# Kernel optimization log

Measured on AMD Instinct MI355X. Metric: run time of the kernel, lower is better.

The kernel has to match this reference:

```python
import jax, jax.numpy as jnp
import numpy as np

B, P1, P2 = 64, 15, 14            # batch, H/patch+1, W/patch
E0, E1, E2 = 8, 8, 8               # embed_dim per mode (512 total)
H1, H2, H3 = 2, 2, 2               # heads per mode (8 heads total)
X, Y, Z = E0 // H1, E1 // H2, E2 // H3  # per-head dims (4,4,4) -> head_dim 64
SCALE = (X * Y * Z) ** -0.5


def tle(x, W0, W1, W2, b):
    # mode-n products on last three modes (ignore_modes=(0,1,2)) + bias
    y = jnp.einsum('bpqxyz,ax->bpqayz', x, W0)
    y = jnp.einsum('bpqayz,cy->bpqacz', y, W1)
    y = jnp.einsum('bpqacz,dz->bpqacd', y, W2)
    return y + b


def split_heads(t):
    b, p, q = t.shape[:3]
    t = t.reshape(b, p, q, X, H1, Y, H2, Z, H3)
    return t.transpose(0, 1, 2, 4, 6, 8, 3, 5, 7)


def attention_core(x, Wq0, Wq1, Wq2, bq, Wk0, Wk1, Wk2, bk,
                   Wv0, Wv1, Wv2, bv, Wo0, Wo1, Wo2, bo):
    Q = split_heads(tle(x, Wq0, Wq1, Wq2, bq))
    K = split_heads(tle(x, Wk0, Wk1, Wk2, bk))
    V = split_heads(tle(x, Wv0, Wv1, Wv2, bv))
    # scores over spatial patch pairs per (h1,h2,h3) head triple
    attn = jnp.einsum('bpqdefxyz,bmndefxyz->bdefpqmn', Q, K) * SCALE
    b, d, e, f, p, q, m, n = attn.shape
    a = jax.nn.softmax(attn.reshape(b, d, e, f, p, q, m * n), axis=-1)
    a = a.reshape(b, d, e, f, p, q, m, n)
    o = jnp.einsum('bdefpqmn,bmndefxyz->bdefpqxyz', a, V)
    # b h1 h2 h3 p q x y z -> b p q (x h1)(y h2)(z h3)
    o = o.transpose(0, 4, 5, 6, 1, 7, 2, 8, 3).reshape(b, p, q, E0, E1, E2)
    return tle(o, Wo0, Wo1, Wo2, bo)


def setup_inputs() -> dict:
    key = jax.random.key(0)
    ks = jax.random.split(key, 17)
    inp = {'x': jax.random.normal(ks[0], (B, P1, P2, E0, E1, E2), jnp.float32)}
    i = 1
    for name in ('q', 'k', 'v', 'o'):
        for mode, dim in enumerate((E0, E1, E2)):
            inp[f'W{name}{mode}'] = jax.random.normal(ks[i], (dim, dim), jnp.float32) * 0.1
            i += 1
        inp[f'b{name}'] = jax.random.normal(ks[i], (E0, E1, E2), jnp.float32) * 0.02
        i += 1
    return inp


def reference(x, Wq0, Wq1, Wq2, bq, Wk0, Wk1, Wk2, bk,
              Wv0, Wv1, Wv2, bv, Wo0, Wo1, Wo2, bo):
    return attention_core(x, Wq0, Wq1, Wq2, bq, Wk0, Wk1, Wk2, bk,
                          Wv0, Wv1, Wv2, bv, Wo0, Wo1, Wo2, bo)
```

## Files before the change

### kernel.cpp

```cpp
#include <hip/hip_runtime.h>

typedef unsigned int   u32;
typedef unsigned short u16;
typedef float f32x16 __attribute__((ext_vector_type(16)));
typedef short s16x8  __attribute__((ext_vector_type(8)));
typedef u32   u32x4  __attribute__((ext_vector_type(4)));
typedef u32   u32x2  __attribute__((ext_vector_type(2)));

#define B_   64
#define P1_  15
#define P2_  14
#define S_   210
#define SP_  224
#define NT_  (B_*S_)
#define E_   512
#define NH_  8
#define HD_  64
#define KSC  0.18033688011112042f

__device__ __forceinline__ u16 f2bf(float f) {
    u32 u = __float_as_uint(f);
    u += 0x7fffu + ((u >> 16) & 1u);
    return (u16)(u >> 16);
}
__device__ __forceinline__ float bf2f(u16 h) {
    return __uint_as_float(((u32)h) << 16);
}
__device__ __forceinline__ u32 cvtpk(float lo, float hi) {
    u32 r;
    asm("v_cvt_pk_bf16_f32 %0, %1, %2" : "=v"(r) : "v"(lo), "v"(hi));
    return r;
}

__device__ __forceinline__ void wfence() {
    asm volatile("s_waitcnt lgkmcnt(0)" ::: "memory");
}

__device__ __forceinline__ void mode_proj(
        const float* xs, float* t1, float* t2,
        const float* __restrict__ W0, const float* __restrict__ W1,
        const float* __restrict__ W2, const float* __restrict__ bb,
        int t, float* y3)
{
    {
        float xv[8];
        #pragma unroll
        for (int i = 0; i < 8; ++i) xv[i] = xs[i*66 + t];
        #pragma unroll
        for (int a = 0; a < 8; ++a) {
            float acc = 0.f;
            #pragma unroll
            for (int i = 0; i < 8; ++i) acc = fmaf(W0[a*8+i], xv[i], acc);
            t1[a*68 + t] = acc;
        }
    }
    wfence();
    {
        const int a = t >> 3, z = t & 7;
        float yv[8];
        #pragma unroll
        for (int y = 0; y < 8; ++y) yv[y] = t1[a*68 + y*8 + z];
        #pragma unroll
        for (int c = 0; c < 8; ++c) {
            float acc = 0.f;
            #pragma unroll
            for (int y = 0; y < 8; ++y) acc = fmaf(W1[c*8+y], yv[y], acc);
            t2[(a*8 + c)*9 + z] = acc;
        }
    }
    wfence();
    {
        float zv[8];
        #pragma unroll
        for (int z = 0; z < 8; ++z) zv[z] = t2[t*9 + z];
        #pragma unroll
        for (int d = 0; d < 8; ++d) {
            float acc = bb[t*8 + d];
            #pragma unroll
            for (int z = 0; z < 8; ++z) acc = fmaf(W2[d*8+z], zv[z], acc);
            y3[d] = acc;
        }
    }
    wfence();
}

__global__ __launch_bounds__(512) void k_qkv(
    const float* __restrict__ x,
    const float* __restrict__ Wq0, const float* __restrict__ Wq1,
    const float* __restrict__ Wq2, const float* __restrict__ bq,
    const float* __restrict__ Wk0, const float* __restrict__ Wk1,
    const float* __restrict__ Wk2, const float* __restrict__ bk,
    const float* __restrict__ Wv0, const float* __restrict__ Wv1,
    const float* __restrict__ Wv2, const float* __restrict__ bv,
    u16* __restrict__ Qo, u16* __restrict__ Ko, u16* __restrict__ Vo)
{
    __shared__ float xs[8][528];
    __shared__ float t1[8][544];
    __shared__ float t2[8][576];
    const int w = threadIdx.x >> 6, t = threadIdx.x & 63;
    const int tok = blockIdx.x*8 + w;
    const int b   = tok / S_;
    const int s   = tok - b * S_;

    const float* xp = x + (size_t)tok * E_;
    #pragma unroll
    for (int k4 = 0; k4 < 2; ++k4) {
        const float4 vv = *reinterpret_cast<const float4*>(xp + k4*256 + t*4);
        const int m0 = k4*4 + (t >> 4);
        const int in = (t*4) & 63;
        xs[w][m0*66 + in + 0] = vv.x;
        xs[w][m0*66 + in + 1] = vv.y;
        xs[w][m0*66 + in + 2] = vv.z;
        xs[w][m0*66 + in + 3] = vv.w;
    }
    wfence();

    const int a  = t >> 3, c = t & 7;
    const int x_ = a >> 1, h1 = a & 1;
    const int y_ = c >> 1, h2 = c & 1;

    float y3[8];

    mode_proj(xs[w], t1[w], t2[w], Wq0, Wq1, Wq2, bq, t, y3);
    #pragma unroll
    for (int h3 = 0; h3 < 2; ++h3) {
        const int h = (((h1 << 1) | h2) << 1) | h3;
        u32x2 pk;
        pk[0] = cvtpk(y3[0 + h3], y3[2 + h3]);
        pk[1] = cvtpk(y3[4 + h3], y3[6 + h3]);
        *reinterpret_cast<u32x2*>(
            Qo + ((size_t)(b*NH_ + h)*SP_ + s)*HD_ + (x_*16 + y_*4)) = pk;
    }
    mode_proj(xs[w], t1[w], t2[w], Wk0, Wk1, Wk2, bk, t, y3);
    #pragma unroll
    for (int h3 = 0; h3 < 2; ++h3) {
        const int h = (((h1 << 1) | h2) << 1) | h3;
        u32x2 pk;
        pk[0] = cvtpk(y3[0 + h3], y3[2 + h3]);
        pk[1] = cvtpk(y3[4 + h3], y3[6 + h3]);
        *reinterpret_cast<u32x2*>(
            Ko + ((size_t)(b*NH_ + h)*SP_ + s)*HD_ + (x_*16 + y_*4)) = pk;
    }
    mode_proj(xs[w], t1[w], t2[w], Wv0, Wv1, Wv2, bv, t, y3);
    #pragma unroll
    for (int h3 = 0; h3 < 2; ++h3) {
        const int h = (((h1 << 1) | h2) << 1) | h3;
        u32x2 pk;
        pk[0] = cvtpk(y3[0 + h3], y3[2 + h3]);
        pk[1] = cvtpk(y3[4 + h3], y3[6 + h3]);
        *reinterpret_cast<u32x2*>(
            Vo + ((size_t)(b*NH_ + h)*SP_ + s)*HD_ + (x_*16 + y_*4)) = pk;
    }
}

__global__ __launch_bounds__(512, 2) void k_attn(
    const u16* __restrict__ Q, const u16* __restrict__ K,
    const u16* __restrict__ V, u16* __restrict__ O)
{
    __shared__ u16   Kl[SP_*64];
    __shared__ u16   Vt[64*232];
    __shared__ float invl[8*32];

    const int bh  = blockIdx.x;
    const int tid = threadIdx.x;
    const u16* Qg = Q + (size_t)bh*SP_*HD_;
    const u16* Kg = K + (size_t)bh*SP_*HD_;
    const u16* Vg = V + (size_t)bh*SP_*HD_;

    const int w    = tid >> 6;
    const int lane = tid & 63;
    const int l31  = lane & 31;
    const int hi   = lane >> 5;
    const int strip = (w < 7) ? w : 6;

    const u16* qb = Qg + (size_t)(strip*32 + l31)*64 + hi*8;
    const s16x8 qf0 = *(const s16x8*)(qb +  0);
    const s16x8 qf1 = *(const s16x8*)(qb + 16);
    const s16x8 qf2 = *(const s16x8*)(qb + 32);
    const s16x8 qf3 = *(const s16x8*)(qb + 48);

    #pragma unroll
    for (int i = 0; i < 4; ++i) {
        int sIdx = i*512 + tid;
        if (sIdx < 1792) {
            int row = sIdx >> 3, cc = sIdx & 7;
            u32x4 d = *(const u32x4*)(Kg + sIdx*8);
            *(u32x4*)&Kl[row*64 + (cc ^ (row & 7))*8] = d;
        }
    }
    if (tid < 448) {
        int tokg = tid >> 3, dg = tid & 7;
        int t0 = tokg*4, d0 = dg*8;
        u32x4 r0 = *(const u32x4*)(Vg + (size_t)(t0+0)*64 + d0);
        u32x4 r1 = *(const u32x4*)(Vg + (size_t)(t0+1)*64 + d0);
        u32x4 r2 = *(const u32x4*)(Vg + (size_t)(t0+2)*64 + d0);
        u32x4 r3 = *(const u32x4*)(Vg + (size_t)(t0+3)*64 + d0);
        #pragma unroll
        for (int j = 0; j < 8; ++j) {
            u32 sel = (j & 1) ? 0x07060302u : 0x05040100u;
            u32 lo  = __builtin_amdgcn_perm(r1[j>>1], r0[j>>1], sel);
            u32 hi2 = __builtin_amdgcn_perm(r3[j>>1], r2[j>>1], sel);
            *(u32x2*)&Vt[(d0+j)*232 + t0] = (u32x2){lo, hi2};
        }
    }
    __syncthreads();

    if (w >= 7) return;

    f32x16 oacc0 = {}, oacc1 = {};
    float  psum  = 0.f;
    const int swz = l31 & 7;

    #pragma unroll
    for (int kt = 0; kt < 7; ++kt) {
        const u16* kbase = &Kl[(kt*32 + l31)*64];
        f32x16 sacc = {};
        s16x8 kf0 = *(const s16x8*)(kbase + ((0 + hi) ^ swz)*8);
        s16x8 kf1 = *(const s16x8*)(kbase + ((2 + hi) ^ swz)*8);
        s16x8 kf2 = *(const s16x8*)(kbase + ((4 + hi) ^ swz)*8);
        s16x8 kf3 = *(const s16x8*)(kbase + ((6 + hi) ^ swz)*8);
        __builtin_amdgcn_s_setprio(1);
        sacc = __builtin_amdgcn_mfma_f32_32x32x16_bf16(kf0, qf0, sacc, 0, 0, 0);
        sacc = __builtin_amdgcn_mfma_f32_32x32x16_bf16(kf1, qf1, sacc, 0, 0, 0);
        sacc = __builtin_amdgcn_mfma_f32_32x32x16_bf16(kf2, qf2, sacc, 0, 0, 0);
        sacc = __builtin_amdgcn_mfma_f32_32x32x16_bf16(kf3, qf3, sacc, 0, 0, 0);
        __builtin_amdgcn_s_setprio(0);

        float p[16];
        #pragma unroll
        for (int r = 0; r < 16; ++r) p[r] = exp2f(sacc[r] * KSC);
        if (kt == 6) {
            const float hm = hi ? 0.f : 1.f;
            p[8] *= hm; p[9] *= hm;
            p[10] = 0.f; p[11] = 0.f; p[12] = 0.f; p[13] = 0.f; p[14] = 0.f; p[15] = 0.f;
        }
        #pragma unroll
        for (int r = 0; r < 16; ++r) psum += p[r];

        u32 c0, c1, c2, c3, c4, c5, c6, c7;
        asm("v_cvt_pk_bf16_f32 %0, %1, %2" : "=v"(c0) : "v"(p[0]),  "v"(p[1]));
        asm("v_cvt_pk_bf16_f32 %0, %1, %2" : "=v"(c1) : "v"(p[2]),  "v"(p[3]));
        asm("v_cvt_pk_bf16_f32 %0, %1, %2" : "=v"(c2) : "v"(p[4]),  "v"(p[5]));
        asm("v_cvt_pk_bf16_f32 %0, %1, %2" : "=v"(c3) : "v"(p[6]),  "v"(p[7]));
        asm("v_cvt_pk_bf16_f32 %0, %1, %2" : "=v"(c4) : "v"(p[8]),  "v"(p[9]));
        asm("v_cvt_pk_bf16_f32 %0, %1, %2" : "=v"(c5) : "v"(p[10]), "v"(p[11]));
        asm("v_cvt_pk_bf16_f32 %0, %1, %2" : "=v"(c6) : "v"(p[12]), "v"(p[13]));
        asm("v_cvt_pk_bf16_f32 %0, %1, %2" : "=v"(c7) : "v"(p[14]), "v"(p[15]));
        asm("v_permlane32_swap_b32 %0, %1" : "+v"(c0), "+v"(c2));
        asm("v_permlane32_swap_b32 %0, %1" : "+v"(c1), "+v"(c3));
        asm("v_permlane32_swap_b32 %0, %1" : "+v"(c4), "+v"(c6));
        asm("v_permlane32_swap_b32 %0, %1" : "+v"(c5), "+v"(c7));
        const s16x8 pf0 = __builtin_bit_cast(s16x8, (u32x4){c0, c1, c2, c3});
        const s16x8 pf1 = __builtin_bit_cast(s16x8, (u32x4){c4, c5, c6, c7});

        const u16* vb = &Vt[kt*32 + hi*8];
        s16x8 vf0 = *(const s16x8*)(vb + (0*32 + l31)*232 +  0);
        s16x8 vf1 = *(const s16x8*)(vb + (0*32 + l31)*232 + 16);
        s16x8 vf2 = *(const s16x8*)(vb + (1*32 + l31)*232 +  0);
        s16x8 vf3 = *(const s16x8*)(vb + (1*32 + l31)*232 + 16);
        __builtin_amdgcn_s_setprio(1);
        oacc0 = __builtin_amdgcn_mfma_f32_32x32x16_bf16(pf0, vf0, oacc0, 0, 0, 0);
        oacc0 = __builtin_amdgcn_mfma_f32_32x32x16_bf16(pf1, vf1, oacc0, 0, 0, 0);
        oacc1 = __builtin_amdgcn_mfma_f32_32x32x16_bf16(pf0, vf2, oacc1, 0, 0, 0);
        oacc1 = __builtin_amdgcn_mfma_f32_32x32x16_bf16(pf1, vf3, oacc1, 0, 0, 0);
        __builtin_amdgcn_s_setprio(0);
    }

    float tot = psum + __shfl_xor(psum, 32, 64);
    invl[w*32 + l31] = 1.0f / tot;
    asm volatile("s_waitcnt lgkmcnt(0)" ::: "memory");

    u16* Ob = O + ((size_t)bh*S_ + strip*32)*HD_;
    #pragma unroll
    for (int r = 0; r < 16; ++r) {
        const int q = (r & 3) + 8*(r >> 2) + 4*hi;
        if (strip == 6 && q >= 18) continue;
        const float iv = invl[w*32 + q];
        Ob[(size_t)q*64 + l31]      = f2bf(oacc0[r] * iv);
        Ob[(size_t)q*64 + 32 + l31] = f2bf(oacc1[r] * iv);
    }
}

__global__ __launch_bounds__(512) void k_oproj(
    const u16* __restrict__ O,
    const float* __restrict__ Wo0, const float* __restrict__ Wo1,
    const float* __restrict__ Wo2, const float* __restrict__ bo,
    float* __restrict__ out)
{
    __shared__ float xs[8][528];
    __shared__ float t1[8][544];
    __shared__ float t2[8][576];
    const int w = threadIdx.x >> 6, t = threadIdx.x & 63;
    const int tok = blockIdx.x*8 + w;
    const int b   = tok / S_;
    const int s   = tok - b * S_;

    const int a  = t >> 3, c = t & 7;
    const int x_ = a >> 1, h1 = a & 1;
    const int y_ = c >> 1, h2 = c & 1;
    #pragma unroll
    for (int h3 = 0; h3 < 2; ++h3) {
        const int h = (((h1 << 1) | h2) << 1) | h3;
        const ushort4 v = *reinterpret_cast<const ushort4*>(
            O + ((size_t)(b*NH_ + h)*S_ + s)*HD_ + (x_*16 + y_*4));
        xs[w][a*66 + c*8 + 0 + h3] = bf2f(v.x);
        xs[w][a*66 + c*8 + 2 + h3] = bf2f(v.y);
        xs[w][a*66 + c*8 + 4 + h3] = bf2f(v.z);
        xs[w][a*66 + c*8 + 6 + h3] = bf2f(v.w);
    }
    wfence();

    float y3[8];
    mode_proj(xs[w], t1[w], t2[w], Wo0, Wo1, Wo2, bo, t, y3);

    float4* op = reinterpret_cast<float4*>(out + (size_t)tok * E_ + t * 8);
    float4 u0, u1;
    u0.x = y3[0]; u0.y = y3[1]; u0.z = y3[2]; u0.w = y3[3];
    u1.x = y3[4]; u1.y = y3[5]; u1.z = y3[6]; u1.w = y3[7];
    op[0] = u0;
    op[1] = u1;
}

extern "C" void kernel_launch(void* const* d_in, const int* in_sizes, int n_in,
                              void* d_out, int out_size, void* d_ws, size_t ws_size,
                              hipStream_t stream)
{
    const float* x   = (const float*)d_in[0];
    const float* Wq0 = (const float*)d_in[1];
    const float* Wq1 = (const float*)d_in[2];
    const float* Wq2 = (const float*)d_in[3];
    const float* bq  = (const float*)d_in[4];
    const float* Wk0 = (const float*)d_in[5];
    const float* Wk1 = (const float*)d_in[6];
    const float* Wk2 = (const float*)d_in[7];
    const float* bk  = (const float*)d_in[8];
    const float* Wv0 = (const float*)d_in[9];
    const float* Wv1 = (const float*)d_in[10];
    const float* Wv2 = (const float*)d_in[11];
    const float* bv  = (const float*)d_in[12];
    const float* Wo0 = (const float*)d_in[13];
    const float* Wo1 = (const float*)d_in[14];
    const float* Wo2 = (const float*)d_in[15];
    const float* bo  = (const float*)d_in[16];

    const size_t TP = (size_t)B_ * NH_ * SP_ * HD_;
    u16* Qs = (u16*)d_ws;
    u16* Ks = Qs + TP;
    u16* Vs = Ks + TP;
    u16* Os = Vs + TP;

    k_qkv<<<NT_/8, 512, 0, stream>>>(x, Wq0, Wq1, Wq2, bq,
                                     Wk0, Wk1, Wk2, bk,
                                     Wv0, Wv1, Wv2, bv, Qs, Ks, Vs);
    k_attn<<<B_*NH_, 512, 0, stream>>>(Qs, Ks, Vs, Os);
    k_oproj<<<NT_/8, 512, 0, stream>>>(Os, Wo0, Wo1, Wo2, bo, (float*)d_out);
}
```

Measured before the change: 152.9 us.

## Fuse QKV, attention and output projection into one cooperative persistent kernel

```diff
diff --git a/kernel.cpp b/kernel.cpp
--- a/kernel.cpp
+++ b/kernel.cpp
@@ -1,4 +1,7 @@
 #include <hip/hip_runtime.h>
+#include <hip/hip_cooperative_groups.h>
+
+namespace cg = cooperative_groups;
 
 typedef unsigned int   u32;
 typedef unsigned short u16;
@@ -18,6 +21,9 @@
 #define HD_  64
 #define KSC  0.18033688011112042f
 
+#define NBLK 256
+#define TPB  512
+
 __device__ __forceinline__ u16 f2bf(float f) {
     u32 u = __float_as_uint(f);
     u += 0x7fffu + ((u >> 16) & 1u);
@@ -84,274 +90,282 @@
     wfence();
 }
 
-__global__ __launch_bounds__(512) void k_qkv(
-    const float* __restrict__ x,
-    const float* __restrict__ Wq0, const float* __restrict__ Wq1,
-    const float* __restrict__ Wq2, const float* __restrict__ bq,
-    const float* __restrict__ Wk0, const float* __restrict__ Wk1,
-    const float* __restrict__ Wk2, const float* __restrict__ bk,
-    const float* __restrict__ Wv0, const float* __restrict__ Wv1,
-    const float* __restrict__ Wv2, const float* __restrict__ bv,
-    u16* __restrict__ Qo, u16* __restrict__ Ko, u16* __restrict__ Vo)
+struct KParams {
+    const float *x;
+    const float *Wq0, *Wq1, *Wq2, *bq;
+    const float *Wk0, *Wk1, *Wk2, *bk;
+    const float *Wv0, *Wv1, *Wv2, *bv;
+    const float *Wo0, *Wo1, *Wo2, *bo;
+    u16 *Qs, *Ks, *Vs, *Os;
+    float *out;
+};
+
+
+__global__ __launch_bounds__(TPB, 4) void k_fused(KParams p)
 {
-    __shared__ float xs[8][528];
-    __shared__ float t1[8][544];
-    __shared__ float t2[8][576];
-    const int w = threadIdx.x >> 6, t = threadIdx.x & 63;
-    const int tok = blockIdx.x*8 + w;
-    const int b   = tok / S_;
-    const int s   = tok - b * S_;
-
-    const float* xp = x + (size_t)tok * E_;
-    #pragma unroll
-    for (int k4 = 0; k4 < 2; ++k4) {
-        const float4 vv = *reinterpret_cast<const float4*>(xp + k4*256 + t*4);
-        const int m0 = k4*4 + (t >> 4);
-        const int in = (t*4) & 63;
-        xs[w][m0*66 + in + 0] = vv.x;
-        xs[w][m0*66 + in + 1] = vv.y;
-        xs[w][m0*66 + in + 2] = vv.z;
-        xs[w][m0*66 + in + 3] = vv.w;
-    }
-    wfence();
-
-    const int a  = t >> 3, c = t & 7;
-    const int x_ = a >> 1, h1 = a & 1;
-    const int y_ = c >> 1, h2 = c & 1;
-
-    float y3[8];
-
-    mode_proj(xs[w], t1[w], t2[w], Wq0, Wq1, Wq2, bq, t, y3);
-    #pragma unroll
-    for (int h3 = 0; h3 < 2; ++h3) {
-        const int h = (((h1 << 1) | h2) << 1) | h3;
-        u32x2 pk;
-        pk[0] = cvtpk(y3[0 + h3], y3[2 + h3]);
-        pk[1] = cvtpk(y3[4 + h3], y3[6 + h3]);
-        *reinterpret_cast<u32x2*>(
-            Qo + ((size_t)(b*NH_ + h)*SP_ + s)*HD_ + (x_*16 + y_*4)) = pk;
-    }
-    mode_proj(xs[w], t1[w], t2[w], Wk0, Wk1, Wk2, bk, t, y3);
-    #pragma unroll
-    for (int h3 = 0; h3 < 2; ++h3) {
-        const int h = (((h1 << 1) | h2) << 1) | h3;
-        u32x2 pk;
-        pk[0] = cvtpk(y3[0 + h3], y3[2 + h3]);
-        pk[1] = cvtpk(y3[4 + h3], y3[6 + h3]);
-        *reinterpret_cast<u32x2*>(
-            Ko + ((size_t)(b*NH_ + h)*SP_ + s)*HD_ + (x_*16 + y_*4)) = pk;
-    }
-    mode_proj(xs[w], t1[w], t2[w], Wv0, Wv1, Wv2, bv, t, y3);
-    #pragma unroll
-    for (int h3 = 0; h3 < 2; ++h3) {
-        const int h = (((h1 << 1) | h2) << 1) | h3;
-        u32x2 pk;
-        pk[0] = cvtpk(y3[0 + h3], y3[2 + h3]);
-        pk[1] = cvtpk(y3[4 + h3], y3[6 + h3]);
-        *reinterpret_cast<u32x2*>(
-            Vo + ((size_t)(b*NH_ + h)*SP_ + s)*HD_ + (x_*16 + y_*4)) = pk;
-    }
-}
-
-__global__ __launch_bounds__(512, 2) void k_attn(
-    const u16* __restrict__ Q, const u16* __restrict__ K,
-    const u16* __restrict__ V, u16* __restrict__ O)
-{
-    __shared__ u16   Kl[SP_*64];
-    __shared__ u16   Vt[64*232];
-    __shared__ float invl[8*32];
-
-    const int bh  = blockIdx.x;
-    const int tid = threadIdx.x;
-    const u16* Qg = Q + (size_t)bh*SP_*HD_;
-    const u16* Kg = K + (size_t)bh*SP_*HD_;
-    const u16* Vg = V + (size_t)bh*SP_*HD_;
-
+    __shared__ __align__(16) char smem[59392];
+    cg::grid_group grid = cg::this_grid();
+
+    const int bid  = blockIdx.x;
+    const int tid  = threadIdx.x;
     const int w    = tid >> 6;
-    const int lane = tid & 63;
-    const int l31  = lane & 31;
-    const int hi   = lane >> 5;
-    const int strip = (w < 7) ? w : 6;
-
-    const u16* qb = Qg + (size_t)(strip*32 + l31)*64 + hi*8;
-    const s16x8 qf0 = *(const s16x8*)(qb +  0);
-    const s16x8 qf1 = *(const s16x8*)(qb + 16);
-    const s16x8 qf2 = *(const s16x8*)(qb + 32);
-    const s16x8 qf3 = *(const s16x8*)(qb + 48);
-
-    #pragma unroll
-    for (int i = 0; i < 4; ++i) {
-        int sIdx = i*512 + tid;
-        if (sIdx < 1792) {
-            int row = sIdx >> 3, cc = sIdx & 7;
-            u32x4 d = *(const u32x4*)(Kg + sIdx*8);
-            *(u32x4*)&Kl[row*64 + (cc ^ (row & 7))*8] = d;
-        }
-    }
-    if (tid < 448) {
-        int tokg = tid >> 3, dg = tid & 7;
-        int t0 = tokg*4, d0 = dg*8;
-        u32x4 r0 = *(const u32x4*)(Vg + (size_t)(t0+0)*64 + d0);
-        u32x4 r1 = *(const u32x4*)(Vg + (size_t)(t0+1)*64 + d0);
-        u32x4 r2 = *(const u32x4*)(Vg + (size_t)(t0+2)*64 + d0);
-        u32x4 r3 = *(const u32x4*)(Vg + (size_t)(t0+3)*64 + d0);
-        #pragma unroll
-        for (int j = 0; j < 8; ++j) {
-            u32 sel = (j & 1) ? 0x07060302u : 0x05040100u;
-            u32 lo  = __builtin_amdgcn_perm(r1[j>>1], r0[j>>1], sel);
-            u32 hi2 = __builtin_amdgcn_perm(r3[j>>1], r2[j>>1], sel);
-            *(u32x2*)&Vt[(d0+j)*232 + t0] = (u32x2){lo, hi2};
-        }
-    }
-    __syncthreads();
-
-    if (w >= 7) return;
-
-    f32x16 oacc0 = {}, oacc1 = {};
-    float  psum  = 0.f;
-    const int swz = l31 & 7;
-
-    #pragma unroll
-    for (int kt = 0; kt < 7; ++kt) {
-        const u16* kbase = &Kl[(kt*32 + l31)*64];
-        f32x16 sacc = {};
-        s16x8 kf0 = *(const s16x8*)(kbase + ((0 + hi) ^ swz)*8);
-        s16x8 kf1 = *(const s16x8*)(kbase + ((2 + hi) ^ swz)*8);
-        s16x8 kf2 = *(const s16x8*)(kbase + ((4 + hi) ^ swz)*8);
-        s16x8 kf3 = *(const s16x8*)(kbase + ((6 + hi) ^ swz)*8);
-        __builtin_amdgcn_s_setprio(1);
-        sacc = __builtin_amdgcn_mfma_f32_32x32x16_bf16(kf0, qf0, sacc, 0, 0, 0);
-        sacc = __builtin_amdgcn_mfma_f32_32x32x16_bf16(kf1, qf1, sacc, 0, 0, 0);
-        sacc = __builtin_amdgcn_mfma_f32_32x32x16_bf16(kf2, qf2, sacc, 0, 0, 0);
-        sacc = __builtin_amdgcn_mfma_f32_32x32x16_bf16(kf3, qf3, sacc, 0, 0, 0);
-        __builtin_amdgcn_s_setprio(0);
-
-        float p[16];
-        #pragma unroll
-        for (int r = 0; r < 16; ++r) p[r] = exp2f(sacc[r] * KSC);
-        if (kt == 6) {
-            const float hm = hi ? 0.f : 1.f;
-            p[8] *= hm; p[9] *= hm;
-            p[10] = 0.f; p[11] = 0.f; p[12] = 0.f; p[13] = 0.f; p[14] = 0.f; p[15] = 0.f;
-        }
-        #pragma unroll
-        for (int r = 0; r < 16; ++r) psum += p[r];
-
-        u32 c0, c1, c2, c3, c4, c5, c6, c7;
-        asm("v_cvt_pk_bf16_f32 %0, %1, %2" : "=v"(c0) : "v"(p[0]),  "v"(p[1]));
-        asm("v_cvt_pk_bf16_f32 %0, %1, %2" : "=v"(c1) : "v"(p[2]),  "v"(p[3]));
-        asm("v_cvt_pk_bf16_f32 %0, %1, %2" : "=v"(c2) : "v"(p[4]),  "v"(p[5]));
-        asm("v_cvt_pk_bf16_f32 %0, %1, %2" : "=v"(c3) : "v"(p[6]),  "v"(p[7]));
-        asm("v_cvt_pk_bf16_f32 %0, %1, %2" : "=v"(c4) : "v"(p[8]),  "v"(p[9]));
-        asm("v_cvt_pk_bf16_f32 %0, %1, %2" : "=v"(c5) : "v"(p[10]), "v"(p[11]));
-        asm("v_cvt_pk_bf16_f32 %0, %1, %2" : "=v"(c6) : "v"(p[12]), "v"(p[13]));
-        asm("v_cvt_pk_bf16_f32 %0, %1, %2" : "=v"(c7) : "v"(p[14]), "v"(p[15]));
-        asm("v_permlane32_swap_b32 %0, %1" : "+v"(c0), "+v"(c2));
-        asm("v_permlane32_swap_b32 %0, %1" : "+v"(c1), "+v"(c3));
-        asm("v_permlane32_swap_b32 %0, %1" : "+v"(c4), "+v"(c6));
-        asm("v_permlane32_swap_b32 %0, %1" : "+v"(c5), "+v"(c7));
-        const s16x8 pf0 = __builtin_bit_cast(s16x8, (u32x4){c0, c1, c2, c3});
-        const s16x8 pf1 = __builtin_bit_cast(s16x8, (u32x4){c4, c5, c6, c7});
-
-        const u16* vb = &Vt[kt*32 + hi*8];
-        s16x8 vf0 = *(const s16x8*)(vb + (0*32 + l31)*232 +  0);
-        s16x8 vf1 = *(const s16x8*)(vb + (0*32 + l31)*232 + 16);
-        s16x8 vf2 = *(const s16x8*)(vb + (1*32 + l31)*232 +  0);
-        s16x8 vf3 = *(const s16x8*)(vb + (1*32 + l31)*232 + 16);
-        __builtin_amdgcn_s_setprio(1);
-        oacc0 = __builtin_amdgcn_mfma_f32_32x32x16_bf16(pf0, vf0, oacc0, 0, 0, 0);
-        oacc0 = __builtin_amdgcn_mfma_f32_32x32x16_bf16(pf1, vf1, oacc0, 0, 0, 0);
-        oacc1 = __builtin_amdgcn_mfma_f32_32x32x16_bf16(pf0, vf2, oacc1, 0, 0, 0);
-        oacc1 = __builtin_amdgcn_mfma_f32_32x32x16_bf16(pf1, vf3, oacc1, 0, 0, 0);
-        __builtin_amdgcn_s_setprio(0);
-    }
-
-    float tot = psum + __shfl_xor(psum, 32, 64);
-    invl[w*32 + l31] = 1.0f / tot;
-    asm volatile("s_waitcnt lgkmcnt(0)" ::: "memory");
-
-    u16* Ob = O + ((size_t)bh*S_ + strip*32)*HD_;
-    #pragma unroll
-    for (int r = 0; r < 16; ++r) {
-        const int q = (r & 3) + 8*(r >> 2) + 4*hi;
-        if (strip == 6 && q >= 18) continue;
-        const float iv = invl[w*32 + q];
-        Ob[(size_t)q*64 + l31]      = f2bf(oacc0[r] * iv);
-        Ob[(size_t)q*64 + 32 + l31] = f2bf(oacc1[r] * iv);
-    }
-}
-
-__global__ __launch_bounds__(512) void k_oproj(
-    const u16* __restrict__ O,
-    const float* __restrict__ Wo0, const float* __restrict__ Wo1,
-    const float* __restrict__ Wo2, const float* __restrict__ bo,
-    float* __restrict__ out)
-{
-    __shared__ float xs[8][528];
-    __shared__ float t1[8][544];
-    __shared__ float t2[8][576];
-    const int w = threadIdx.x >> 6, t = threadIdx.x & 63;
-    const int tok = blockIdx.x*8 + w;
-    const int b   = tok / S_;
-    const int s   = tok - b * S_;
-
-    const int a  = t >> 3, c = t & 7;
-    const int x_ = a >> 1, h1 = a & 1;
-    const int y_ = c >> 1, h2 = c & 1;
-    #pragma unroll
-    for (int h3 = 0; h3 < 2; ++h3) {
-        const int h = (((h1 << 1) | h2) << 1) | h3;
-        const ushort4 v = *reinterpret_cast<const ushort4*>(
-            O + ((size_t)(b*NH_ + h)*S_ + s)*HD_ + (x_*16 + y_*4));
-        xs[w][a*66 + c*8 + 0 + h3] = bf2f(v.x);
-        xs[w][a*66 + c*8 + 2 + h3] = bf2f(v.y);
-        xs[w][a*66 + c*8 + 4 + h3] = bf2f(v.z);
-        xs[w][a*66 + c*8 + 6 + h3] = bf2f(v.w);
-    }
-    wfence();
-
-    float y3[8];
-    mode_proj(xs[w], t1[w], t2[w], Wo0, Wo1, Wo2, bo, t, y3);
-
-    float4* op = reinterpret_cast<float4*>(out + (size_t)tok * E_ + t * 8);
-    float4 u0, u1;
-    u0.x = y3[0]; u0.y = y3[1]; u0.z = y3[2]; u0.w = y3[3];
-    u1.x = y3[4]; u1.y = y3[5]; u1.z = y3[6]; u1.w = y3[7];
-    op[0] = u0;
-    op[1] = u1;
+    const int t    = tid & 63;
+
+    {
+        float* xs = (float*)smem;
+        float* t1 = (float*)(smem + 16896);
+        float* t2 = (float*)(smem + 34304);
+        const int a  = t >> 3, c = t & 7;
+        const int x_ = a >> 1, h1 = a & 1;
+        const int y_ = c >> 1, h2 = c & 1;
+
+        for (int it = 0; it < 7; ++it) {
+            const int tok = it*2048 + bid*8 + w;
+            if (tok >= NT_) break;
+            const int b = tok / S_;
+            const int s = tok - b * S_;
+
+            const float* xp = p.x + (size_t)tok * E_;
+            #pragma unroll
+            for (int k4 = 0; k4 < 2; ++k4) {
+                const float4 vv = *reinterpret_cast<const float4*>(xp + k4*256 + t*4);
+                const int m0 = k4*4 + (t >> 4);
+                const int in = (t*4) & 63;
+                xs[w*528 + m0*66 + in + 0] = vv.x;
+                xs[w*528 + m0*66 + in + 1] = vv.y;
+                xs[w*528 + m0*66 + in + 2] = vv.z;
+                xs[w*528 + m0*66 + in + 3] = vv.w;
+            }
+            wfence();
+
+            float y3[8];
+            mode_proj(xs + w*528, t1 + w*544, t2 + w*576, p.Wq0, p.Wq1, p.Wq2, p.bq, t, y3);
+            #pragma unroll
+            for (int h3 = 0; h3 < 2; ++h3) {
+                const int h = (((h1 << 1) | h2) << 1) | h3;
+                u32x2 pk;
+                pk[0] = cvtpk(y3[0 + h3], y3[2 + h3]);
+                pk[1] = cvtpk(y3[4 + h3], y3[6 + h3]);
+                *reinterpret_cast<u32x2*>(
+                    p.Qs + ((size_t)(b*NH_ + h)*SP_ + s)*HD_ + (x_*16 + y_*4)) = pk;
+            }
+            mode_proj(xs + w*528, t1 + w*544, t2 + w*576, p.Wk0, p.Wk1, p.Wk2, p.bk, t, y3);
+            #pragma unroll
+            for (int h3 = 0; h3 < 2; ++h3) {
+                const int h = (((h1 << 1) | h2) << 1) | h3;
+                u32x2 pk;
+                pk[0] = cvtpk(y3[0 + h3], y3[2 + h3]);
+                pk[1] = cvtpk(y3[4 + h3], y3[6 + h3]);
+                *reinterpret_cast<u32x2*>(
+                    p.Ks + ((size_t)(b*NH_ + h)*SP_ + s)*HD_ + (x_*16 + y_*4)) = pk;
+            }
+            mode_proj(xs + w*528, t1 + w*544, t2 + w*576, p.Wv0, p.Wv1, p.Wv2, p.bv, t, y3);
+            #pragma unroll
+            for (int h3 = 0; h3 < 2; ++h3) {
+                const int h = (((h1 << 1) | h2) << 1) | h3;
+                u32x2 pk;
+                pk[0] = cvtpk(y3[0 + h3], y3[2 + h3]);
+                pk[1] = cvtpk(y3[4 + h3], y3[6 + h3]);
+                *reinterpret_cast<u32x2*>(
+                    p.Vs + ((size_t)(b*NH_ + h)*SP_ + s)*HD_ + (x_*16 + y_*4)) = pk;
+            }
+        }
+    }
+
+    __threadfence();
+    grid.sync();
+
+    {
+        u16*   Kl   = (u16*)smem;
+        u16*   Vt   = (u16*)(smem + 28672);
+        float* invl = (float*)(smem + 58368);
+
+        const int lane = tid & 63;
+        const int l31  = lane & 31;
+        const int hi   = lane >> 5;
+        const int strip = (w < 7) ? w : 6;
+
+        for (int rep = 0; rep < 2; ++rep) {
+            if (rep) __syncthreads();
+            const int bh = bid + rep*256;
+            const u16* Qg = p.Qs + (size_t)bh*SP_*HD_;
+            const u16* Kg = p.Ks + (size_t)bh*SP_*HD_;
+            const u16* Vg = p.Vs + (size_t)bh*SP_*HD_;
+
+            const u16* qb = Qg + (size_t)(strip*32 + l31)*64 + hi*8;
+            const s16x8 qf0 = *(const s16x8*)(qb +  0);
+            const s16x8 qf1 = *(const s16x8*)(qb + 16);
+            const s16x8 qf2 = *(const s16x8*)(qb + 32);
+            const s16x8 qf3 = *(const s16x8*)(qb + 48);
+
+            #pragma unroll
+            for (int i = 0; i < 4; ++i) {
+                int sIdx = i*512 + tid;
+                if (sIdx < 1792) {
+                    int row = sIdx >> 3, cc = sIdx & 7;
+                    u32x4 d = *(const u32x4*)(Kg + sIdx*8);
+                    *(u32x4*)&Kl[row*64 + (cc ^ (row & 7))*8] = d;
+                }
+            }
+            if (tid < 448) {
+                int tokg = tid >> 3, dg = tid & 7;
+                int t0 = tokg*4, d0 = dg*8;
+                u32x4 r0 = *(const u32x4*)(Vg + (size_t)(t0+0)*64 + d0);
+                u32x4 r1 = *(const u32x4*)(Vg + (size_t)(t0+1)*64 + d0);
+                u32x4 r2 = *(const u32x4*)(Vg + (size_t)(t0+2)*64 + d0);
+                u32x4 r3 = *(const u32x4*)(Vg + (size_t)(t0+3)*64 + d0);
+                #pragma unroll
+                for (int j = 0; j < 8; ++j) {
+                    u32 sel = (j & 1) ? 0x07060302u : 0x05040100u;
+                    u32 lo  = __builtin_amdgcn_perm(r1[j>>1], r0[j>>1], sel);
+                    u32 hi2 = __builtin_amdgcn_perm(r3[j>>1], r2[j>>1], sel);
+                    *(u32x2*)&Vt[(d0+j)*232 + t0] = (u32x2){lo, hi2};
+                }
+            }
+            __syncthreads();
+
+            if (w < 7) {
+                f32x16 oacc0 = {}, oacc1 = {};
+                float  psum  = 0.f;
+                const int swz = l31 & 7;
+
+                #pragma unroll
+                for (int kt = 0; kt < 7; ++kt) {
+                    const u16* kbase = &Kl[(kt*32 + l31)*64];
+                    f32x16 sacc = {};
+                    s16x8 kf0 = *(const s16x8*)(kbase + ((0 + hi) ^ swz)*8);
+                    s16x8 kf1 = *(const s16x8*)(kbase + ((2 + hi) ^ swz)*8);
+                    s16x8 kf2 = *(const s16x8*)(kbase + ((4 + hi) ^ swz)*8);
+                    s16x8 kf3 = *(const s16x8*)(kbase + ((6 + hi) ^ swz)*8);
+                    __builtin_amdgcn_s_setprio(1);
+                    sacc = __builtin_amdgcn_mfma_f32_32x32x16_bf16(kf0, qf0, sacc, 0, 0, 0);
+                    sacc = __builtin_amdgcn_mfma_f32_32x32x16_bf16(kf1, qf1, sacc, 0, 0, 0);
+                    sacc = __builtin_amdgcn_mfma_f32_32x32x16_bf16(kf2, qf2, sacc, 0, 0, 0);
+                    sacc = __builtin_amdgcn_mfma_f32_32x32x16_bf16(kf3, qf3, sacc, 0, 0, 0);
+                    __builtin_amdgcn_s_setprio(0);
+
+                    float pr[16];
+                    #pragma unroll
+                    for (int r = 0; r < 16; ++r) pr[r] = exp2f(sacc[r] * KSC);
+                    if (kt == 6) {
+                        const float hm = hi ? 0.f : 1.f;
+                        pr[8] *= hm; pr[9] *= hm;
+                        pr[10] = 0.f; pr[11] = 0.f; pr[12] = 0.f; pr[13] = 0.f; pr[14] = 0.f; pr[15] = 0.f;
+                    }
+                    #pragma unroll
+                    for (int r = 0; r < 16; ++r) psum += pr[r];
+
+                    u32 c0, c1, c2, c3, c4, c5, c6, c7;
+                    asm("v_cvt_pk_bf16_f32 %0, %1, %2" : "=v"(c0) : "v"(pr[0]),  "v"(pr[1]));
+                    asm("v_cvt_pk_bf16_f32 %0, %1, %2" : "=v"(c1) : "v"(pr[2]),  "v"(pr[3]));
+                    asm("v_cvt_pk_bf16_f32 %0, %1, %2" : "=v"(c2) : "v"(pr[4]),  "v"(pr[5]));
+                    asm("v_cvt_pk_bf16_f32 %0, %1, %2" : "=v"(c3) : "v"(pr[6]),  "v"(pr[7]));
+                    asm("v_cvt_pk_bf16_f32 %0, %1, %2" : "=v"(c4) : "v"(pr[8]),  "v"(pr[9]));
+                    asm("v_cvt_pk_bf16_f32 %0, %1, %2" : "=v"(c5) : "v"(pr[10]), "v"(pr[11]));
+                    asm("v_cvt_pk_bf16_f32 %0, %1, %2" : "=v"(c6) : "v"(pr[12]), "v"(pr[13]));
+                    asm("v_cvt_pk_bf16_f32 %0, %1, %2" : "=v"(c7) : "v"(pr[14]), "v"(pr[15]));
+                    asm("v_permlane32_swap_b32 %0, %1" : "+v"(c0), "+v"(c2));
+                    asm("v_permlane32_swap_b32 %0, %1" : "+v"(c1), "+v"(c3));
+                    asm("v_permlane32_swap_b32 %0, %1" : "+v"(c4), "+v"(c6));
+                    asm("v_permlane32_swap_b32 %0, %1" : "+v"(c5), "+v"(c7));
+                    const s16x8 pf0 = __builtin_bit_cast(s16x8, (u32x4){c0, c1, c2, c3});
+                    const s16x8 pf1 = __builtin_bit_cast(s16x8, (u32x4){c4, c5, c6, c7});
+
+                    const u16* vb = &Vt[kt*32 + hi*8];
+                    s16x8 vf0 = *(const s16x8*)(vb + (0*32 + l31)*232 +  0);
+                    s16x8 vf1 = *(const s16x8*)(vb + (0*32 + l31)*232 + 16);
+                    s16x8 vf2 = *(const s16x8*)(vb + (1*32 + l31)*232 +  0);
+                    s16x8 vf3 = *(const s16x8*)(vb + (1*32 + l31)*232 + 16);
+                    __builtin_amdgcn_s_setprio(1);
+                    oacc0 = __builtin_amdgcn_mfma_f32_32x32x16_bf16(pf0, vf0, oacc0, 0, 0, 0);
+                    oacc0 = __builtin_amdgcn_mfma_f32_32x32x16_bf16(pf1, vf1, oacc0, 0, 0, 0);
+                    oacc1 = __builtin_amdgcn_mfma_f32_32x32x16_bf16(pf0, vf2, oacc1, 0, 0, 0);
+                    oacc1 = __builtin_amdgcn_mfma_f32_32x32x16_bf16(pf1, vf3, oacc1, 0, 0, 0);
+                    __builtin_amdgcn_s_setprio(0);
+                }
+
+                float tot = psum + __shfl_xor(psum, 32, 64);
+                invl[w*32 + l31] = 1.0f / tot;
+                wfence();
+
+                u16* Ob = p.Os + ((size_t)bh*S_ + strip*32)*HD_;
+                #pragma unroll
+                for (int r = 0; r < 16; ++r) {
+                    const int q = (r & 3) + 8*(r >> 2) + 4*hi;
+                    if (strip == 6 && q >= 18) continue;
+                    const float iv = invl[w*32 + q];
+                    Ob[(size_t)q*64 + l31]      = f2bf(oacc0[r] * iv);
+                    Ob[(size_t)q*64 + 32 + l31] = f2bf(oacc1[r] * iv);
+                }
+            }
+        }
+    }
+
+    __threadfence();
+    grid.sync();
+
+    {
+        float* xs = (float*)smem;
+        float* t1 = (float*)(smem + 16896);
+        float* t2 = (float*)(smem + 34304);
+        const int a  = t >> 3, c = t & 7;
+        const int x_ = a >> 1, h1 = a & 1;
+        const int y_ = c >> 1, h2 = c & 1;
+
+        for (int it = 0; it < 7; ++it) {
+            const int tok = it*2048 + bid*8 + w;
+            if (tok >= NT_) break;
+            const int b = tok / S_;
+            const int s = tok - b * S_;
+
+            #pragma unroll
+            for (int h3 = 0; h3 < 2; ++h3) {
+                const int h = (((h1 << 1) | h2) << 1) | h3;
+                const ushort4 v = *reinterpret_cast<const ushort4*>(
+                    p.Os + ((size_t)(b*NH_ + h)*S_ + s)*HD_ + (x_*16 + y_*4));
+                xs[w*528 + a*66 + c*8 + 0 + h3] = bf2f(v.x);
+                xs[w*528 + a*66 + c*8 + 2 + h3] = bf2f(v.y);
+                xs[w*528 + a*66 + c*8 + 4 + h3] = bf2f(v.z);
+                xs[w*528 + a*66 + c*8 + 6 + h3] = bf2f(v.w);
+            }
+            wfence();
+
+            float y3[8];
+            mode_proj(xs + w*528, t1 + w*544, t2 + w*576, p.Wo0, p.Wo1, p.Wo2, p.bo, t, y3);
+
+            float4* op = reinterpret_cast<float4*>(p.out + (size_t)tok * E_ + t * 8);
+            float4 u0, u1;
+            u0.x = y3[0]; u0.y = y3[1]; u0.z = y3[2]; u0.w = y3[3];
+            u1.x = y3[4]; u1.y = y3[5]; u1.z = y3[6]; u1.w = y3[7];
+            op[0] = u0;
+            op[1] = u1;
+        }
+    }
 }
 
 extern "C" void kernel_launch(void* const* d_in, const int* in_sizes, int n_in,
                               void* d_out, int out_size, void* d_ws, size_t ws_size,
                               hipStream_t stream)
 {
-    const float* x   = (const float*)d_in[0];
-    const float* Wq0 = (const float*)d_in[1];
-    const float* Wq1 = (const float*)d_in[2];
-    const float* Wq2 = (const float*)d_in[3];
-    const float* bq  = (const float*)d_in[4];
-    const float* Wk0 = (const float*)d_in[5];
-    const float* Wk1 = (const float*)d_in[6];
-    const float* Wk2 = (const float*)d_in[7];
-    const float* bk  = (const float*)d_in[8];
-    const float* Wv0 = (const float*)d_in[9];
-    const float* Wv1 = (const float*)d_in[10];
-    const float* Wv2 = (const float*)d_in[11];
-    const float* bv  = (const float*)d_in[12];
-    const float* Wo0 = (const float*)d_in[13];
-    const float* Wo1 = (const float*)d_in[14];
-    const float* Wo2 = (const float*)d_in[15];
-    const float* bo  = (const float*)d_in[16];
-
     const size_t TP = (size_t)B_ * NH_ * SP_ * HD_;
-    u16* Qs = (u16*)d_ws;
-    u16* Ks = Qs + TP;
-    u16* Vs = Ks + TP;
-    u16* Os = Vs + TP;
-
-    k_qkv<<<NT_/8, 512, 0, stream>>>(x, Wq0, Wq1, Wq2, bq,
-                                     Wk0, Wk1, Wk2, bk,
-                                     Wv0, Wv1, Wv2, bv, Qs, Ks, Vs);
-    k_attn<<<B_*NH_, 512, 0, stream>>>(Qs, Ks, Vs, Os);
-    k_oproj<<<NT_/8, 512, 0, stream>>>(Os, Wo0, Wo1, Wo2, bo, (float*)d_out);
-}
+
+    KParams p;
+    p.x   = (const float*)d_in[0];
+    p.Wq0 = (const float*)d_in[1];  p.Wq1 = (const float*)d_in[2];
+    p.Wq2 = (const float*)d_in[3];  p.bq  = (const float*)d_in[4];
+    p.Wk0 = (const float*)d_in[5];  p.Wk1 = (const float*)d_in[6];
+    p.Wk2 = (const float*)d_in[7];  p.bk  = (const float*)d_in[8];
+    p.Wv0 = (const float*)d_in[9];  p.Wv1 = (const float*)d_in[10];
+    p.Wv2 = (const float*)d_in[11]; p.bv  = (const float*)d_in[12];
+    p.Wo0 = (const float*)d_in[13]; p.Wo1 = (const float*)d_in[14];
+    p.Wo2 = (const float*)d_in[15]; p.bo  = (const float*)d_in[16];
+    p.Qs  = (u16*)d_ws;
+    p.Ks  = p.Qs + TP;
+    p.Vs  = p.Ks + TP;
+    p.Os  = p.Vs + TP;
+    p.out = (float*)d_out;
+
+    void* args[] = { &p };
+    hipLaunchCooperativeKernel((const void*)k_fused,
+                               dim3(NBLK), dim3(TPB), args, 0, stream);
+}
```

Result: slower. 406.1 us (+165.5%).
